# Optimization experiments

Measured on AMD Instinct MI355X. Metric: run time of the kernel, lower is better.

Reference implementation:

```python
import jax, jax.numpy as jnp
import numpy as np

B, T, C, HEAD = 4, 4096, 2048, 128
ROPE_BASE = 10000.0


def _rope_tables(T, dim):
    # precompute_freqs_cis: freqs = 1/base^(2i/dim), angles = t * freqs
    inv_freq = 1.0 / (ROPE_BASE ** (np.arange(0, dim, 2, dtype=np.float32) / dim))
    angles = np.arange(T, dtype=np.float32)[:, None] * inv_freq[None, :]  # [T, dim/2]
    return jnp.asarray(np.cos(angles)), jnp.asarray(np.sin(angles))


def _apply_rope(x, cos, sin):
    # x: [B, T, D]; interleaved complex pairs (x[2i], x[2i+1]) rotated by angle
    B_, T_, D = x.shape
    xr = x.reshape(B_, T_, D // 2, 2)
    x1, x2 = xr[..., 0], xr[..., 1]
    o1 = x1 * cos - x2 * sin
    o2 = x1 * sin + x2 * cos
    return jnp.stack([o1, o2], axis=-1).reshape(B_, T_, D)


def setup_inputs() -> dict:
    key0 = jax.random.key(0)
    k1, k2, k3, k4 = jax.random.split(key0, 4)
    x = jax.random.normal(k1, (B, T, C), dtype=jnp.float32)
    key = jax.random.normal(k2, (B, T, HEAD), dtype=jnp.float32)
    value = jax.random.normal(k3, (B, T, HEAD), dtype=jnp.float32)
    w_q = jax.random.normal(k4, (HEAD, C), dtype=jnp.float32) * 0.02
    return {"x": x, "key": key, "value": value, "w_q": w_q}


def reference(x, key, value, w_q):
    # query projection (nn.Linear, no bias)
    q = jnp.einsum('btc,dc->btd', x, w_q)  # [B, T, HEAD]
    cos, sin = _rope_tables(T, HEAD)
    # apply_rotary_emb(key, query) returns (key_rot, query_rot); then
    # query, key = (key_rot, query_rot) and wei = key @ query^T == q_rot @ k_rot^T
    q_rot = _apply_rope(q, cos, sin)
    k_rot = _apply_rope(key, cos, sin)
    scale = HEAD ** -0.5
    wei = jnp.einsum('btd,bsd->bts', q_rot, k_rot) * scale  # [B, T, T]
    causal = jnp.tril(jnp.ones((T, T), dtype=bool))
    wei = jnp.where(causal, wei, -jnp.inf)
    wei = jax.nn.softmax(wei, axis=-1)
    # dropout is identity in eval / p=0
    return jnp.einsum('bts,bsd->btd', wei, value)  # [B, T, HEAD]
```

## Files before the change

### kernel.cpp

```cpp
#include <hip/hip_runtime.h>
#include <hip/hip_bf16.h>

#define TSEQ  4096
#define NBATCH 4
#define CDIM  2048
#define DH    128

typedef __bf16 bf16x8 __attribute__((ext_vector_type(8)));
typedef float  f32x4  __attribute__((ext_vector_type(4)));
typedef unsigned short u16x8 __attribute__((ext_vector_type(8)));
typedef unsigned       u32x4 __attribute__((ext_vector_type(4)));
typedef unsigned short u16;

__device__ __forceinline__ u16 f2bf(float f) {
  union { float f; unsigned u; } v; v.f = f;
  unsigned r = (v.u + 0x7FFFu + ((v.u >> 16) & 1u)) >> 16;
  return (u16)r;
}
__device__ __forceinline__ float bf2f(u16 h) {
  union { unsigned u; float f; } v; v.u = ((unsigned)h) << 16;
  return v.f;
}
__device__ __forceinline__ bf16x8 ld_bf8(const u16* p) {
  return __builtin_bit_cast(bf16x8, *(const u16x8*)p);
}
__device__ __forceinline__ unsigned pk2(float lo, float hi) {
  float2 f; f.x = lo; f.y = hi;
  __hip_bfloat162 h = __float22bfloat162_rn(f);
  unsigned r; __builtin_memcpy(&r, &h, 4);
  return r;
}
__device__ __forceinline__ u16x8 cvt8u(float4 a, float4 b) {
  u32x4 u;
  u[0] = pk2(a.x, a.y); u[1] = pk2(a.z, a.w);
  u[2] = pk2(b.x, b.y); u[3] = pk2(b.z, b.w);
  return __builtin_bit_cast(u16x8, u);
}

__device__ __forceinline__ void lds_barrier() {
  asm volatile("s_waitcnt lgkmcnt(0)" ::: "memory");
  __builtin_amdgcn_s_barrier();
}

template<int CTRL>
__device__ __forceinline__ float dppmv(float x) {
  return __builtin_bit_cast(float,
    __builtin_amdgcn_update_dpp(0, __builtin_bit_cast(int, x), CTRL, 0xF, 0xF, true));
}
__device__ __forceinline__ float red_max16(float v) {
  v = fmaxf(v, dppmv<0xB1>(v));
  v = fmaxf(v, dppmv<0x4E>(v));
  v = fmaxf(v, dppmv<0x124>(v));
  v = fmaxf(v, dppmv<0x128>(v));
  return v;
}
__device__ __forceinline__ float red_sum16(float v) {
  v += dppmv<0xB1>(v);
  v += dppmv<0x4E>(v);
  v += dppmv<0x124>(v);
  v += dppmv<0x128>(v);
  return v;
}

__device__ __forceinline__ int unit_base(int Q) {
  int a = Q >> 2, bq = Q & 3;
  return 2 * a * (a + 1) + bq * (a + 1);
}

__global__ __launch_bounds__(256) void k_prep(const float* __restrict__ w, u16* __restrict__ wbf,
                                              const float* __restrict__ key, u16* __restrict__ krot,
                                              const float* __restrict__ value, u16* __restrict__ vt) {
  __shared__ u16 S[128 * 66];
  int bid = blockIdx.x;
  int tid = threadIdx.x;
  if (bid < 256) {
    int vb = bid;
    int b = vb >> 6;
    int t0 = (vb & 63) * 64;
    int d = (tid & 31) * 4;
    int tl0 = tid >> 5;
#pragma unroll
    for (int i = 0; i < 8; ++i) {
      int tl = tl0 + i * 8;
      const float4 val = *(const float4*)(value + ((size_t)(b * TSEQ + t0 + tl)) * DH + d);
      S[(d + 0) * 66 + tl] = f2bf(val.x);
      S[(d + 1) * 66 + tl] = f2bf(val.y);
      S[(d + 2) * 66 + tl] = f2bf(val.z);
      S[(d + 3) * 66 + tl] = f2bf(val.w);
    }
    __syncthreads();
#pragma unroll
    for (int i = 0; i < 16; ++i) {
      int idx = tid + i * 256;
      int dd = idx >> 5;
      int tw = (idx & 31) * 2;
      unsigned lo = S[dd * 66 + tw];
      unsigned hi = S[dd * 66 + tw + 1];
      *(unsigned*)(vt + ((size_t)(b * DH + dd)) * TSEQ + t0 + tw) = lo | (hi << 16);
    }
  } else if (bid < 512) {
    int i = (bid - 256) * 256 + tid;
    const float4 v = *(const float4*)(w + (size_t)i * 4);
    uint2 o; o.x = pk2(v.x, v.y); o.y = pk2(v.z, v.w);
    *(uint2*)(wbf + (size_t)i * 4) = o;
  } else {
    int g = (bid - 512) * 256 + tid;
    int p = g & 63;
    int row = g >> 6;
    int t = row & (TSEQ - 1);
    const float2 kv = *(const float2*)(key + (size_t)row * DH + 2 * p);
    float inv = powf(10000.0f, -(float)p / 64.0f);
    float ang = (float)t * inv;
    float s, c; sincosf(ang, &s, &c);
    *(unsigned*)(krot + (size_t)row * DH + 2 * p) = pk2(kv.x * c - kv.y * s, kv.x * s + kv.y * c);
  }
}

__global__ __launch_bounds__(256, 2) void k_qproj(const float* __restrict__ x,
                                                  const u16* __restrict__ wbf,
                                                  u16* __restrict__ qrot) {
  __shared__ u16 Al[16 * 32 * 8];
  int bid = blockIdx.x;
  int tid = threadIdx.x;
  int w = tid >> 6;
  int lane = tid & 63;
  int l15 = lane & 15;
  int quad = lane >> 4;
  int m0 = bid * 32;

  int srow = tid >> 3;
  int c16 = (tid & 7) * 16;
  int chunk0 = (tid & 7) * 2;
  const float* xg = x + (size_t)(m0 + srow) * CDIM + c16;

  f32x4 acc[2][2];
#pragma unroll
  for (int mt = 0; mt < 2; ++mt)
#pragma unroll
    for (int nt = 0; nt < 2; ++nt) acc[mt][nt] = (f32x4){0.f, 0.f, 0.f, 0.f};

  float4 paA[4], paB[4];
#pragma unroll
  for (int i = 0; i < 4; ++i) paA[i] = *(const float4*)(xg + i * 4);
#pragma unroll
  for (int i = 0; i < 4; ++i) paB[i] = *(const float4*)(xg + 128 + i * 4);

  auto qstep = [&](float4 (&pa)[4], int itc) {
    u16x8 lo = cvt8u(pa[0], pa[1]);
    u16x8 hi = cvt8u(pa[2], pa[3]);
    if (itc + 2 < CDIM / 128) {
      const float* xn = xg + (size_t)(itc + 2) * 128;
#pragma unroll
      for (int i = 0; i < 4; ++i) pa[i] = *(const float4*)(xn + i * 4);
    }
    lds_barrier();
    *(u16x8*)&Al[(chunk0 * 32 + srow) * 8] = lo;
    *(u16x8*)&Al[((chunk0 + 1) * 32 + srow) * 8] = hi;
    lds_barrier();
    int k0 = itc * 128;
#pragma unroll
    for (int ks = 0; ks < 4; ++ks) {
      bf16x8 af[2];
#pragma unroll
      for (int mt = 0; mt < 2; ++mt)
        af[mt] = ld_bf8(&Al[(((ks * 4 + quad) * 32) + mt * 16 + l15) * 8]);
#pragma unroll
      for (int nt = 0; nt < 2; ++nt) {
        bf16x8 bfrag = ld_bf8(wbf + (size_t)(w * 32 + nt * 16 + l15) * CDIM + k0 + ks * 32 + quad * 8);
#pragma unroll
        for (int mt = 0; mt < 2; ++mt)
          acc[mt][nt] = __builtin_amdgcn_mfma_f32_16x16x32_bf16(af[mt], bfrag, acc[mt][nt], 0, 0, 0);
      }
    }
  };

#pragma unroll 1
  for (int ith = 0; ith < 8; ++ith) {
    qstep(paA, 2 * ith);
    qstep(paB, 2 * ith + 1);
  }

  const float scale = 0.08838834764831845f;
#pragma unroll
  for (int nt = 0; nt < 2; ++nt) {
    int dcol = w * 32 + nt * 16 + l15;
    int p = dcol >> 1;
    float inv = powf(10000.0f, -(float)p / 64.0f);
#pragma unroll
    for (int mt = 0; mt < 2; ++mt) {
#pragma unroll
      for (int r = 0; r < 4; ++r) {
        int m = m0 + mt * 16 + quad * 4 + r;
        int t = m & (TSEQ - 1);
        float ang = (float)t * inv;
        float s, c; sincosf(ang, &s, &c);
        float val = acc[mt][nt][r];
        float partner = __shfl_xor(val, 1, 64);
        float o = (lane & 1) ? (val * c + partner * s) : (val * c - partner * s);
        qrot[(size_t)m * DH + dcol] = f2bf(o * scale);
      }
    }
  }
}

__global__ __launch_bounds__(256, 2) void k_attn(const u16* __restrict__ qrot,
                                                 const u16* __restrict__ krot,
                                                 const u16* __restrict__ vt,
                                                 u16* __restrict__ Opart,
                                                 float2* __restrict__ ml) {
  __shared__ u16 Kl[16 * 64 * 8];
  __shared__ u16 Vl[8 * 128 * 8];
  __shared__ u16 Pl[4 * 32 * 72];

  int bid = blockIdx.x;
  int b = bid / 144;
  int u = bid - b * 144;
  int Q = 0;
#pragma unroll 1
  for (int q = 31; q >= 0; --q) {
    if (unit_base(q) <= u) { Q = q; break; }
  }
  int kc = u - unit_base(Q);
  int nkt = 2 * Q + 2;
  int kt0 = kc * 8;
  int kt1 = min(kt0 + 8, nkt);
  int m0 = Q * 128;

  int tid = threadIdx.x;
  int w = tid >> 6;
  int lane = tid & 63;
  int l15 = lane & 15;
  int quad = lane >> 4;
  u16* pw = Pl + w * 32 * 72;

  int rK = tid & 63;   int jgK = tid >> 6;
  int dV = tid & 127;  int hV = tid >> 7;

  const u16* kb = krot + (size_t)b * TSEQ * DH;
  const u16* vb = vt + (size_t)b * DH * TSEQ;

  bf16x8 qf[2][4];
#pragma unroll
  for (int mt = 0; mt < 2; ++mt) {
    const u16* qb = qrot + ((size_t)(b * TSEQ + m0 + mt * 64 + w * 16 + l15)) * DH + quad * 8;
#pragma unroll
    for (int c = 0; c < 4; ++c) qf[mt][c] = ld_bf8(qb + c * 32);
  }

  f32x4 o_acc[2][8];
#pragma unroll
  for (int mt = 0; mt < 2; ++mt)
#pragma unroll
    for (int i = 0; i < 8; ++i) o_acc[mt][i] = (f32x4){0.f, 0.f, 0.f, 0.f};
  float m_st[2][4], l_st[2][4];
#pragma unroll
  for (int mt = 0; mt < 2; ++mt)
#pragma unroll
    for (int r = 0; r < 4; ++r) { m_st[mt][r] = -INFINITY; l_st[mt][r] = 0.f; }

  u16x8 kr[4], vr[4];
  {
    const u16* ks = kb + (size_t)(kt0 * 64 + rK) * DH + jgK * 32;
    const u16* vs = vb + (size_t)dV * TSEQ + kt0 * 64 + hV * 32;
#pragma unroll
    for (int i = 0; i < 4; ++i) { kr[i] = *(const u16x8*)(ks + i * 8); vr[i] = *(const u16x8*)(vs + i * 8); }
  }

  for (int kt = kt0; kt < kt1; ++kt) {
    lds_barrier();
#pragma unroll
    for (int i = 0; i < 4; ++i) {
      *(u16x8*)&Kl[((jgK * 4 + i) * 64 + rK) * 8] = kr[i];
      *(u16x8*)&Vl[((hV * 4 + i) * 128 + dV) * 8] = vr[i];
    }
    lds_barrier();
    if (kt + 1 < kt1) {
      const u16* ks = kb + (size_t)((kt + 1) * 64 + rK) * DH + jgK * 32;
      const u16* vs = vb + (size_t)dV * TSEQ + (kt + 1) * 64 + hV * 32;
#pragma unroll
      for (int i = 0; i < 4; ++i) { kr[i] = *(const u16x8*)(ks + i * 8); vr[i] = *(const u16x8*)(vs + i * 8); }
    }

    f32x4 s[2][4];
#pragma unroll
    for (int mt = 0; mt < 2; ++mt)
#pragma unroll
      for (int nt = 0; nt < 4; ++nt) s[mt][nt] = (f32x4){0.f, 0.f, 0.f, 0.f};
    __builtin_amdgcn_s_setprio(1);
#pragma unroll
    for (int c = 0; c < 4; ++c)
#pragma unroll
      for (int nt = 0; nt < 4; ++nt) {
        bf16x8 kf = ld_bf8(&Kl[((c * 4 + quad) * 64 + nt * 16 + l15) * 8]);
#pragma unroll
        for (int mt = 0; mt < 2; ++mt)
          s[mt][nt] = __builtin_amdgcn_mfma_f32_16x16x32_bf16(qf[mt][c], kf, s[mt][nt], 0, 0, 0);
      }
    __builtin_amdgcn_s_setprio(0);

    if (kt * 64 >= m0) {
#pragma unroll
      for (int mt = 0; mt < 2; ++mt)
#pragma unroll
        for (int nt = 0; nt < 4; ++nt)
#pragma unroll
          for (int r = 0; r < 4; ++r) {
            int key_g = kt * 64 + nt * 16 + l15;
            int row_g = m0 + mt * 64 + w * 16 + quad * 4 + r;
            if (key_g > row_g) s[mt][nt][r] = -INFINITY;
          }
    }

    float alpha[2][4];
    int chg = 0;
#pragma unroll
    for (int mt = 0; mt < 2; ++mt)
#pragma unroll
      for (int r = 0; r < 4; ++r) {
        float rm = fmaxf(fmaxf(s[mt][0][r], s[mt][1][r]), fmaxf(s[mt][2][r], s[mt][3][r]));
        rm = red_max16(rm);
        float mn = fmaxf(m_st[mt][r], rm);
        float al = __expf(m_st[mt][r] - mn);
        m_st[mt][r] = mn;
        float ps = 0.f;
#pragma unroll
        for (int nt = 0; nt < 4; ++nt) {
          float pv = __expf(s[mt][nt][r] - mn);
          s[mt][nt][r] = pv;
          ps += pv;
        }
        ps = red_sum16(ps);
        l_st[mt][r] = l_st[mt][r] * al + ps;
        alpha[mt][r] = al;
        chg |= (al != 1.0f);
      }
    if (__any(chg)) {
#pragma unroll
      for (int mt = 0; mt < 2; ++mt)
#pragma unroll
        for (int nt = 0; nt < 8; ++nt)
#pragma unroll
          for (int r = 0; r < 4; ++r) o_acc[mt][nt][r] *= alpha[mt][r];
    }

#pragma unroll
    for (int mt = 0; mt < 2; ++mt)
#pragma unroll
      for (int nt = 0; nt < 4; ++nt)
#pragma unroll
        for (int r = 0; r < 4; ++r)
          pw[(mt * 16 + quad * 4 + r) * 72 + nt * 16 + l15] = f2bf(s[mt][nt][r]);

#pragma unroll
    for (int c2 = 0; c2 < 2; ++c2) {
      bf16x8 pf[2];
#pragma unroll
      for (int mt = 0; mt < 2; ++mt)
        pf[mt] = ld_bf8(pw + (mt * 16 + l15) * 72 + c2 * 32 + quad * 8);
      __builtin_amdgcn_s_setprio(1);
#pragma unroll
      for (int nt = 0; nt < 8; ++nt) {
        bf16x8 vf = ld_bf8(&Vl[((c2 * 4 + quad) * 128 + nt * 16 + l15) * 8]);
#pragma unroll
        for (int mt = 0; mt < 2; ++mt)
          o_acc[mt][nt] = __builtin_amdgcn_mfma_f32_16x16x32_bf16(pf[mt], vf, o_acc[mt][nt], 0, 0, 0);
      }
      __builtin_amdgcn_s_setprio(0);
    }
  }

  u16* op = Opart + (size_t)bid * (128 * 128);
#pragma unroll
  for (int mt = 0; mt < 2; ++mt)
#pragma unroll
    for (int nt = 0; nt < 8; ++nt)
#pragma unroll
      for (int r = 0; r < 4; ++r)
        op[(mt * 64 + w * 16 + quad * 4 + r) * 128 + nt * 16 + l15] = f2bf(o_acc[mt][nt][r]);
  if (l15 == 0) {
#pragma unroll
    for (int mt = 0; mt < 2; ++mt)
#pragma unroll
      for (int r = 0; r < 4; ++r) {
        float2 p; p.x = m_st[mt][r]; p.y = l_st[mt][r];
        ml[(size_t)bid * 128 + mt * 64 + w * 16 + quad * 4 + r] = p;
      }
  }
}

__global__ __launch_bounds__(256) void k_merge(const u16* __restrict__ Opart,
                                               const float2* __restrict__ ml,
                                               float* __restrict__ out) {
  __shared__ float wgt[8][128];
  __shared__ float invL[128];
  int bid = blockIdx.x;
  int b = bid >> 5, Q = bid & 31;
  int C = (Q >> 2) + 1;
  int base = b * 144 + unit_base(Q);
  int tid = threadIdx.x;
  if (tid < 128) {
    float mv[8], lv[8];
    float M = -INFINITY;
    for (int c = 0; c < C; ++c) {
      float2 p = ml[(size_t)(base + c) * 128 + tid];
      mv[c] = p.x; lv[c] = p.y;
      M = fmaxf(M, p.x);
    }
    float L = 0.f;
    for (int c = 0; c < C; ++c) {
      float wv = __expf(mv[c] - M);
      wgt[c][tid] = wv;
      L += wv * lv[c];
    }
    invL[tid] = 1.f / L;
  }
  __syncthreads();
#pragma unroll
  for (int k = 0; k < 8; ++k) {
    int slot = tid + k * 256;
    int row = slot >> 4;
    float acc[8];
#pragma unroll
    for (int j = 0; j < 8; ++j) acc[j] = 0.f;
    for (int c = 0; c < C; ++c) {
      u16x8 v = *(const u16x8*)&Opart[(size_t)(base + c) * (128 * 128) + slot * 8];
      float wv = wgt[c][row];
#pragma unroll
      for (int j = 0; j < 8; ++j) acc[j] += wv * bf2f(v[j]);
    }
    float il = invL[row];
    float4 o0, o1;
    o0.x = acc[0] * il; o0.y = acc[1] * il; o0.z = acc[2] * il; o0.w = acc[3] * il;
    o1.x = acc[4] * il; o1.y = acc[5] * il; o1.z = acc[6] * il; o1.w = acc[7] * il;
    float* op = out + ((size_t)(b * TSEQ + Q * 128 + row)) * DH + (slot & 15) * 8;
    *(float4*)op = o0;
    *(float4*)(op + 4) = o1;
  }
}

extern "C" void kernel_launch(void* const* d_in, const int* in_sizes, int n_in,
                              void* d_out, int out_size, void* d_ws, size_t ws_size,
                              hipStream_t stream) {
  const float* x     = (const float*)d_in[0];
  const float* key   = (const float*)d_in[1];
  const float* value = (const float*)d_in[2];
  const float* w_q   = (const float*)d_in[3];
  float* out = (float*)d_out;

  char* ws = (char*)d_ws;
  u16* wbf    = (u16*)(ws);
  u16* qrot   = (u16*)(ws + (1u  << 20));
  u16* krot   = (u16*)(ws + (5u  << 20));
  u16* vt     = (u16*)(ws + (9u  << 20));
  u16* Opart  = (u16*)(ws + (13u << 20));
  float2* ml  = (float2*)(ws + (32u << 20));

  k_prep<<<4608, 256, 0, stream>>>(w_q, wbf, key, krot, value, vt);
  k_qproj<<<(NBATCH * TSEQ) / 32, 256, 0, stream>>>(x, wbf, qrot);
  k_attn<<<NBATCH * 144, 256, 0, stream>>>(qrot, krot, vt, Opart, ml);
  k_merge<<<NBATCH * 32, 256, 0, stream>>>(Opart, ml, out);
}
```

Before: 292.1 us.

## Fuse prep into qproj kernel and merge into attention via last-block atomic counter

Combines the value-transpose, key RoPE and query projection into a single launch, and has the qproj blocks convert the fp32 weights to bf16 on the fly instead of reading a pre-converted copy. The separate merge kernel goes away: blocks whose query tile has only one key chunk write normalized output directly, and for multi-chunk tiles the last finishing block (found with an atomic counter) does the merge. This cuts launches and intermediate traffic, but adds repeated weight conversion, atomics and thread fences.

```diff
diff --git a/kernel.cpp b/kernel.cpp
--- a/kernel.cpp
+++ b/kernel.cpp
@@ -67,16 +67,22 @@
   return 2 * a * (a + 1) + bq * (a + 1);
 }
 
-__global__ __launch_bounds__(256) void k_prep(const float* __restrict__ w, u16* __restrict__ wbf,
-                                              const float* __restrict__ key, u16* __restrict__ krot,
-                                              const float* __restrict__ value, u16* __restrict__ vt) {
+__global__ __launch_bounds__(256, 2) void k_fused1(const float* __restrict__ w,
+                                                   const float* __restrict__ key,
+                                                   u16* __restrict__ krot,
+                                                   const float* __restrict__ value,
+                                                   u16* __restrict__ vt,
+                                                   const float* __restrict__ x,
+                                                   u16* __restrict__ qrot,
+                                                   int* __restrict__ cnt) {
   __shared__ u16 S[128 * 66];
   int bid = blockIdx.x;
   int tid = threadIdx.x;
+
   if (bid < 256) {
-    int vb = bid;
-    int b = vb >> 6;
-    int t0 = (vb & 63) * 64;
+    if (bid == 0 && tid < 128) cnt[tid] = 0;
+    int b = bid >> 6;
+    int t0 = (bid & 63) * 64;
     int d = (tid & 31) * 4;
     int tl0 = tid >> 5;
 #pragma unroll
@@ -98,35 +104,37 @@
       unsigned hi = S[dd * 66 + tw + 1];
       *(unsigned*)(vt + ((size_t)(b * DH + dd)) * TSEQ + t0 + tw) = lo | (hi << 16);
     }
-  } else if (bid < 512) {
-    int i = (bid - 256) * 256 + tid;
-    const float4 v = *(const float4*)(w + (size_t)i * 4);
-    uint2 o; o.x = pk2(v.x, v.y); o.y = pk2(v.z, v.w);
-    *(uint2*)(wbf + (size_t)i * 4) = o;
-  } else {
-    int g = (bid - 512) * 256 + tid;
-    int p = g & 63;
-    int row = g >> 6;
+    return;
+  }
+
+  if (bid < 2304) {
+    int idx = (bid - 256) * 256 + tid;
+    int f0 = idx * 4;
+    int row = f0 >> 7;
+    int d = f0 & 127;
+    int p = d >> 1;
     int t = row & (TSEQ - 1);
-    const float2 kv = *(const float2*)(key + (size_t)row * DH + 2 * p);
-    float inv = powf(10000.0f, -(float)p / 64.0f);
-    float ang = (float)t * inv;
-    float s, c; sincosf(ang, &s, &c);
-    *(unsigned*)(krot + (size_t)row * DH + 2 * p) = pk2(kv.x * c - kv.y * s, kv.x * s + kv.y * c);
-  }
-}
-
-__global__ __launch_bounds__(256, 2) void k_qproj(const float* __restrict__ x,
-                                                  const u16* __restrict__ wbf,
-                                                  u16* __restrict__ qrot) {
-  __shared__ u16 Al[16 * 32 * 8];
-  int bid = blockIdx.x;
-  int tid = threadIdx.x;
-  int w = tid >> 6;
+    const float4 kv = *(const float4*)(key + (size_t)row * DH + d);
+    float inv0 = powf(10000.0f, -(float)p / 64.0f);
+    float inv1 = powf(10000.0f, -(float)(p + 1) / 64.0f);
+    float s0, c0, s1, c1;
+    sincosf((float)t * inv0, &s0, &c0);
+    sincosf((float)t * inv1, &s1, &c1);
+    uint2 o;
+    o.x = pk2(kv.x * c0 - kv.y * s0, kv.x * s0 + kv.y * c0);
+    o.y = pk2(kv.z * c1 - kv.w * s1, kv.z * s1 + kv.w * c1);
+    *(uint2*)(krot + (size_t)row * DH + d) = o;
+    return;
+  }
+
+  int bid2 = bid - 2304;
+  int wv = tid >> 6;
   int lane = tid & 63;
   int l15 = lane & 15;
   int quad = lane >> 4;
-  int m0 = bid * 32;
+  int m0 = bid2 * 32;
+
+  u16* Al = S;
 
   int srow = tid >> 3;
   int c16 = (tid & 7) * 16;
@@ -166,7 +174,10 @@
         af[mt] = ld_bf8(&Al[(((ks * 4 + quad) * 32) + mt * 16 + l15) * 8]);
 #pragma unroll
       for (int nt = 0; nt < 2; ++nt) {
-        bf16x8 bfrag = ld_bf8(wbf + (size_t)(w * 32 + nt * 16 + l15) * CDIM + k0 + ks * 32 + quad * 8);
+        const float* wp = w + (size_t)(wv * 32 + nt * 16 + l15) * CDIM + k0 + ks * 32 + quad * 8;
+        float4 w0 = *(const float4*)wp;
+        float4 w1 = *(const float4*)(wp + 4);
+        bf16x8 bfrag = __builtin_bit_cast(bf16x8, cvt8u(w0, w1));
 #pragma unroll
         for (int mt = 0; mt < 2; ++mt)
           acc[mt][nt] = __builtin_amdgcn_mfma_f32_16x16x32_bf16(af[mt], bfrag, acc[mt][nt], 0, 0, 0);
@@ -183,7 +194,7 @@
   const float scale = 0.08838834764831845f;
 #pragma unroll
   for (int nt = 0; nt < 2; ++nt) {
-    int dcol = w * 32 + nt * 16 + l15;
+    int dcol = wv * 32 + nt * 16 + l15;
     int p = dcol >> 1;
     float inv = powf(10000.0f, -(float)p / 64.0f);
 #pragma unroll
@@ -207,10 +218,13 @@
                                                  const u16* __restrict__ krot,
                                                  const u16* __restrict__ vt,
                                                  u16* __restrict__ Opart,
-                                                 float2* __restrict__ ml) {
+                                                 float2* __restrict__ ml,
+                                                 int* __restrict__ cnt,
+                                                 float* __restrict__ out) {
   __shared__ u16 Kl[16 * 64 * 8];
   __shared__ u16 Vl[8 * 128 * 8];
   __shared__ u16 Pl[4 * 32 * 72];
+  __shared__ int s_last;
 
   int bid = blockIdx.x;
   int b = bid / 144;
@@ -225,6 +239,7 @@
   int kt0 = kc * 8;
   int kt1 = min(kt0 + 8, nkt);
   int m0 = Q * 128;
+  int C = (Q >> 2) + 1;
 
   int tid = threadIdx.x;
   int w = tid >> 6;
@@ -369,6 +384,21 @@
     }
   }
 
+  if (C == 1) {
+#pragma unroll
+    for (int mt = 0; mt < 2; ++mt)
+#pragma unroll
+      for (int r = 0; r < 4; ++r) {
+        float invl = 1.f / l_st[mt][r];
+        int row = m0 + mt * 64 + w * 16 + quad * 4 + r;
+        float* op = out + ((size_t)(b * TSEQ + row)) * DH;
+#pragma unroll
+        for (int nt = 0; nt < 8; ++nt)
+          op[nt * 16 + l15] = bf2f(f2bf(o_acc[mt][nt][r])) * invl;
+      }
+    return;
+  }
+
   u16* op = Opart + (size_t)bid * (128 * 128);
 #pragma unroll
   for (int mt = 0; mt < 2; ++mt)
@@ -386,32 +416,34 @@
         ml[(size_t)bid * 128 + mt * 64 + w * 16 + quad * 4 + r] = p;
       }
   }
-}
-
-__global__ __launch_bounds__(256) void k_merge(const u16* __restrict__ Opart,
-                                               const float2* __restrict__ ml,
-                                               float* __restrict__ out) {
-  __shared__ float wgt[8][128];
-  __shared__ float invL[128];
-  int bid = blockIdx.x;
-  int b = bid >> 5, Q = bid & 31;
-  int C = (Q >> 2) + 1;
+
+  __threadfence();
+  if (tid == 0) s_last = (atomicAdd(&cnt[b * 32 + Q], 1) == C - 1);
+  __syncthreads();
+  if (!s_last) return;
+  __threadfence();
+
   int base = b * 144 + unit_base(Q);
-  int tid = threadIdx.x;
+  float* wgt = (float*)Kl;
+  float* invL = wgt + 8 * 128;
   if (tid < 128) {
     float mv[8], lv[8];
     float M = -INFINITY;
-    for (int c = 0; c < C; ++c) {
-      float2 p = ml[(size_t)(base + c) * 128 + tid];
-      mv[c] = p.x; lv[c] = p.y;
-      M = fmaxf(M, p.x);
-    }
+#pragma unroll
+    for (int c = 0; c < 8; ++c)
+      if (c < C) {
+        float2 p = ml[(size_t)(base + c) * 128 + tid];
+        mv[c] = p.x; lv[c] = p.y;
+        M = fmaxf(M, p.x);
+      }
     float L = 0.f;
-    for (int c = 0; c < C; ++c) {
-      float wv = __expf(mv[c] - M);
-      wgt[c][tid] = wv;
-      L += wv * lv[c];
-    }
+#pragma unroll
+    for (int c = 0; c < 8; ++c)
+      if (c < C) {
+        float wvv = __expf(mv[c] - M);
+        wgt[c * 128 + tid] = wvv;
+        L += wvv * lv[c];
+      }
     invL[tid] = 1.f / L;
   }
   __syncthreads();
@@ -424,17 +456,17 @@
     for (int j = 0; j < 8; ++j) acc[j] = 0.f;
     for (int c = 0; c < C; ++c) {
       u16x8 v = *(const u16x8*)&Opart[(size_t)(base + c) * (128 * 128) + slot * 8];
-      float wv = wgt[c][row];
-#pragma unroll
-      for (int j = 0; j < 8; ++j) acc[j] += wv * bf2f(v[j]);
+      float wvv = wgt[c * 128 + row];
+#pragma unroll
+      for (int j = 0; j < 8; ++j) acc[j] += wvv * bf2f(v[j]);
     }
     float il = invL[row];
     float4 o0, o1;
     o0.x = acc[0] * il; o0.y = acc[1] * il; o0.z = acc[2] * il; o0.w = acc[3] * il;
     o1.x = acc[4] * il; o1.y = acc[5] * il; o1.z = acc[6] * il; o1.w = acc[7] * il;
-    float* op = out + ((size_t)(b * TSEQ + Q * 128 + row)) * DH + (slot & 15) * 8;
-    *(float4*)op = o0;
-    *(float4*)(op + 4) = o1;
+    float* opt = out + ((size_t)(b * TSEQ + Q * 128 + row)) * DH + (slot & 15) * 8;
+    *(float4*)opt = o0;
+    *(float4*)(opt + 4) = o1;
   }
 }
 
@@ -448,15 +480,13 @@
   float* out = (float*)d_out;
 
   char* ws = (char*)d_ws;
-  u16* wbf    = (u16*)(ws);
-  u16* qrot   = (u16*)(ws + (1u  << 20));
-  u16* krot   = (u16*)(ws + (5u  << 20));
-  u16* vt     = (u16*)(ws + (9u  << 20));
-  u16* Opart  = (u16*)(ws + (13u << 20));
-  float2* ml  = (float2*)(ws + (32u << 20));
-
-  k_prep<<<4608, 256, 0, stream>>>(w_q, wbf, key, krot, value, vt);
-  k_qproj<<<(NBATCH * TSEQ) / 32, 256, 0, stream>>>(x, wbf, qrot);
-  k_attn<<<NBATCH * 144, 256, 0, stream>>>(qrot, krot, vt, Opart, ml);
-  k_merge<<<NBATCH * 32, 256, 0, stream>>>(Opart, ml, out);
-}
+  u16* qrot   = (u16*)(ws);
+  u16* krot   = (u16*)(ws + (4u  << 20));
+  u16* vt     = (u16*)(ws + (8u  << 20));
+  u16* Opart  = (u16*)(ws + (12u << 20));
+  float2* ml  = (float2*)(ws + (31u << 20));
+  int* cnt    = (int*)(ws + (32u << 20));
+
+  k_fused1<<<2816, 256, 0, stream>>>(w_q, key, krot, value, vt, x, qrot, cnt);
+  k_attn<<<NBATCH * 144, 256, 0, stream>>>(qrot, krot, vt, Opart, ml, cnt, out);
+}
```

After: 445.3 us. 1.52x slower.
